# Performance work log

Measured on AMD Instinct MI355X. Metric: run time of the kernel, lower is better.

The kernel has to match this reference:

```python
import math
import jax, jax.numpy as jnp
import numpy as np

HEADS = 8

def relative_shift(score):
    # score: [B, H, S, 2S-1] -> [B, H, S, S] via Music Transformer skew trick
    B, H, S, R = score.shape
    score = jnp.pad(score, ((0, 0), (0, 0), (0, 0), (1, 0)))          # [B,H,S,2S]
    score = score.reshape(B, H, -1)[:, :, S:].reshape(B, H, S, -1)    # [B,H,S,2S-1]
    return score[..., :S]


def setup_inputs() -> dict:
    B, S, D = 4, 1024, 512
    dh = D // HEADS
    rng = jax.random.key(0)
    ks = jax.random.split(rng, 14)
    w = 0.02  # init scale
    return {
        "query":   jax.random.normal(ks[0], (B, S, D), jnp.float32),
        "key":     jax.random.normal(ks[1], (B, S, D), jnp.float32),
        "value":   jax.random.normal(ks[2], (B, S, D), jnp.float32),
        "pos_emb": jax.random.normal(ks[3], (2 * S - 1, dh), jnp.float32),
        "Wq": jax.random.normal(ks[4], (D, D), jnp.float32) * w,
        "bq": jnp.zeros((D,), jnp.float32),
        "Wk": jax.random.normal(ks[5], (D, D), jnp.float32) * w,
        "bk": jnp.zeros((D,), jnp.float32),
        "Wv": jax.random.normal(ks[6], (D, D), jnp.float32) * w,
        "bv": jnp.zeros((D,), jnp.float32),
        "Wo": jax.random.normal(ks[7], (D, D), jnp.float32) * w,
        "bo": jnp.zeros((D,), jnp.float32),
        "Wp": jax.random.normal(ks[8], (dh, dh), jnp.float32) * w,
        "bp": jnp.zeros((dh,), jnp.float32),
    }


def reference(query, key, value, pos_emb, Wq, bq, Wk, bk, Wv, bv, Wo, bo, Wp, bp):
    B, S, D = query.shape
    H = HEADS
    dh = D // H
    q = (query @ Wq.T + bq).reshape(B, S, H, dh).transpose(0, 2, 1, 3)  # [B,H,S,dh]
    k = (key   @ Wk.T + bk).reshape(B, S, H, dh).transpose(0, 2, 1, 3)  # [B,H,S,dh]
    v = (value @ Wv.T + bv).reshape(B, S, H, dh).transpose(0, 2, 1, 3)  # [B,H,S,dh]
    rel = pos_emb @ Wp.T + bp                                           # [2S-1, dh]

    pos_score = jnp.einsum('bhsd,rd->bhsr', q, rel)                     # [B,H,S,2S-1]
    pos_score = relative_shift(pos_score)                               # [B,H,S,S]
    content_score = jnp.einsum('bhsd,bhtd->bhst', q, k)                 # [B,H,S,S]
    score = (content_score + pos_score) / math.sqrt(D)                  # scale by sqrt(d_model)
    attn = jax.nn.softmax(score, axis=-1)
    out = jnp.einsum('bhst,bhtd->bshd', attn, v).reshape(B, S, D)
    return (out @ Wo.T + bo, attn, content_score, pos_score)
```

## Files before the change

### kernel.cpp

```cpp
#include <hip/hip_runtime.h>

typedef __attribute__((ext_vector_type(8))) short short8;
typedef __attribute__((ext_vector_type(4))) float f32x4;
typedef __attribute__((ext_vector_type(2))) float f32x2;
typedef unsigned short u16;
typedef unsigned int u32;

#define MFMA16(a, b, c) __builtin_amdgcn_mfma_f32_16x16x32_bf16((a), (b), (c), 0, 0, 0)
#define SCALE 0.044194173824159216f

#define SW(r, c) ((c) ^ (((r) & 7) << 3))

__device__ __forceinline__ u16 f2bf(float f) {
    u32 u = __float_as_uint(f);
    u = (u + 0x7fffu + ((u >> 16) & 1u)) >> 16;
    return (u16)u;
}

__global__ __launch_bounds__(256) void cvt_kernel(const float* __restrict__ src,
                                                  u16* __restrict__ dst, int n4) {
    int i = blockIdx.x * 256 + threadIdx.x;
    if (i >= n4) return;
    float4 v = ((const float4*)src)[i];
    unsigned long long p = (unsigned long long)f2bf(v.x)
                         | ((unsigned long long)f2bf(v.y) << 16)
                         | ((unsigned long long)f2bf(v.z) << 32)
                         | ((unsigned long long)f2bf(v.w) << 48);
    ((unsigned long long*)dst)[i] = p;
}

__global__ __launch_bounds__(256) void rel_kernel(const float* __restrict__ pos_emb,
                                                  const float* __restrict__ Wp,
                                                  const float* __restrict__ bp,
                                                  u16* __restrict__ rel) {
    int idx = blockIdx.x * 256 + threadIdx.x;
    if (idx >= 2047 * 64) return;
    int r = idx >> 6, c = idx & 63;
    const float* pe = pos_emb + r * 64;
    const float* w  = Wp + c * 64;
    float acc = bp[c];
#pragma unroll
    for (int k = 0; k < 64; k++) acc += pe[k] * w[k];
    rel[r * 64 + c] = f2bf(acc);
}

template <int MODE>
__global__ __launch_bounds__(256) void gemm_kernel(const u16* __restrict__ A,
                                                   const u16* __restrict__ B,
                                                   const float* __restrict__ bias,
                                                   void* __restrict__ Cout,
                                                   int M, int N, int K) {
    int tid = threadIdx.x;
    int w = tid >> 6, lane = tid & 63;
    int wi = w >> 1, wj = w & 1;
    int qd = lane >> 4, ln = lane & 15;
    int m_base = blockIdx.x * 64 + wi * 32;
    int n_base = blockIdx.y * 64 + wj * 32;
    f32x4 acc[2][2] = {};
    const u16* a0p = A + (long)(m_base + ln) * K + qd * 8;
    const u16* a1p = a0p + 16 * K;
    const u16* b0p = B + (long)(n_base + ln) * K + qd * 8;
    const u16* b1p = b0p + 16 * K;
    for (int kc = 0; kc < K; kc += 32) {
        short8 a0 = *(const short8*)(a0p + kc);
        short8 a1 = *(const short8*)(a1p + kc);
        short8 b0 = *(const short8*)(b0p + kc);
        short8 b1 = *(const short8*)(b1p + kc);
        acc[0][0] = MFMA16(a0, b0, acc[0][0]);
        acc[0][1] = MFMA16(a0, b1, acc[0][1]);
        acc[1][0] = MFMA16(a1, b0, acc[1][0]);
        acc[1][1] = MFMA16(a1, b1, acc[1][1]);
    }
#pragma unroll
    for (int i = 0; i < 2; i++)
#pragma unroll
        for (int j = 0; j < 2; j++)
#pragma unroll
            for (int r = 0; r < 4; r++) {
                int m = m_base + i * 16 + qd * 4 + r;
                int n = n_base + j * 16 + ln;
                float v = acc[i][j][r];
                if (MODE == 0) {
                    v += bias[n];
                    int b = m >> 10, s = m & 1023, h = n >> 6, d = n & 63;
                    ((u16*)Cout)[(((long)(b * 8 + h) << 10) + s) * 64 + d] = f2bf(v);
                } else if (MODE == 1) {
                    v += bias[m];
                    int b = n >> 10, t = n & 1023, h = m >> 6, d = m & 63;
                    ((u16*)Cout)[(((long)(b * 8 + h) * 64 + d) << 10) + t] = f2bf(v);
                } else {
                    v += bias[n];
                    ((float*)Cout)[(long)m * N + n] = v;
                }
            }
}

__global__ __launch_bounds__(256) void score_kernel(const u16* __restrict__ qws,
                                                    const u16* __restrict__ kws,
                                                    const u16* __restrict__ vtws,
                                                    const u16* __restrict__ relws,
                                                    float* __restrict__ out_attn,
                                                    float* __restrict__ out_cont,
                                                    float* __restrict__ out_pos,
                                                    u16* __restrict__ ctx,
                                                    float* __restrict__ sinvws) {
    __shared__ __align__(16) u16 sc[32][1024];
    int st = blockIdx.x, h = blockIdx.y, b = blockIdx.z;
    int s0 = st * 32;
    int tid = threadIdx.x;
    int w = tid >> 6, lane = tid & 63, qd = lane >> 4, ln = lane & 15;
    int bh = b * 8 + h;
    int c0 = w * 256;

    const u16* qbase  = qws + ((long)bh << 10) * 64;
    const u16* kbase  = kws + ((long)bh << 10) * 64;
    const u16* vtbase = vtws + ((long)bh << 6) * 1024;
    float* attn_base = out_attn + ((long)bh << 20) + (long)s0 * 1024;
    float* cont_base = out_cont + ((long)bh << 20) + (long)s0 * 1024;
    float* pos_base  = out_pos  + ((long)bh << 20) + (long)s0 * 1024;

    short8 qa00 = *(const short8*)(qbase + (s0 + ln) * 64 + qd * 8);
    short8 qa01 = *(const short8*)(qbase + (s0 + ln) * 64 + 32 + qd * 8);
    short8 qa10 = *(const short8*)(qbase + (s0 + 16 + ln) * 64 + qd * 8);
    short8 qa11 = *(const short8*)(qbase + (s0 + 16 + ln) * 64 + 32 + qd * 8);

    for (int tt = 0; tt < 16; tt++) {
        int t0 = c0 + tt * 16;
        const u16* kp = kbase + (t0 + ln) * 64 + qd * 8;
        short8 kb0 = *(const short8*)(kp);
        short8 kb1 = *(const short8*)(kp + 32);
        f32x4 a0 = {}, a1 = {};
        a0 = MFMA16(qa00, kb0, a0);
        a0 = MFMA16(qa01, kb1, a0);
        a1 = MFMA16(qa10, kb0, a1);
        a1 = MFMA16(qa11, kb1, a1);
        int t = t0 + ln;
#pragma unroll
        for (int r = 0; r < 4; r++) {
            int sl = qd * 4 + r;
            cont_base[sl * 1024 + t] = a0[r];
            cont_base[(sl + 16) * 1024 + t] = a1[r];
            sc[sl][SW(sl, t)] = f2bf(a0[r] * SCALE);
            sc[sl + 16][SW(sl + 16, t)] = f2bf(a1[r] * SCALE);
        }
    }

    int rbase = 1008 - s0;
    for (int rt = 16 * w - 1; rt <= 16 * w + 16; rt++) {
        int r0 = rbase + rt * 16;
        const u16* rp = relws + (r0 + ln) * 64 + qd * 8;
        short8 rb0 = *(const short8*)(rp);
        short8 rb1 = *(const short8*)(rp + 32);
        f32x4 a0 = {}, a1 = {};
        a0 = MFMA16(qa00, rb0, a0);
        a0 = MFMA16(qa01, rb1, a0);
        a1 = MFMA16(qa10, rb0, a1);
        a1 = MFMA16(qa11, rb1, a1);
#pragma unroll
        for (int r = 0; r < 4; r++) {
            int sl = qd * 4 + r;
            int t = rt * 16 + ln + sl - 15;
            if (t >= c0 && t < c0 + 256) {
                pos_base[sl * 1024 + t] = a0[r];
                u16 cur = sc[sl][SW(sl, t)];
                float fv = __uint_as_float((u32)cur << 16) + a0[r] * SCALE;
                sc[sl][SW(sl, t)] = f2bf(fv);
            }
            int t1 = t + 16;
            if (t1 >= c0 && t1 < c0 + 256) {
                pos_base[(sl + 16) * 1024 + t1] = a1[r];
                u16 cur = sc[sl + 16][SW(sl + 16, t1)];
                float fv = __uint_as_float((u32)cur << 16) + a1[r] * SCALE;
                sc[sl + 16][SW(sl + 16, t1)] = f2bf(fv);
            }
        }
    }
    __syncthreads();

    {
        int row = tid >> 3, g = tid & 7;
        float sum = 0.f;
#pragma unroll
        for (int i = 0; i < 64; i++) {
            int c = 2 * g + 16 * i;
            u32 pk = *(const u32*)&sc[row][SW(row, c)];
            float e0 = __expf(__uint_as_float(pk << 16));
            float e1 = __expf(__uint_as_float(pk & 0xffff0000u));
            sum += e0 + e1;
            u32 pe;
            asm("v_cvt_pk_bf16_f32 %0, %1, %2" : "=v"(pe) : "v"(e0), "v"(e1));
            *(u32*)&sc[row][SW(row, c)] = pe;
        }
        sum += __shfl_xor(sum, 1, 8);
        sum += __shfl_xor(sum, 2, 8);
        sum += __shfl_xor(sum, 4, 8);
        float inv = 1.0f / sum;
        if (g == 0) sinvws[((long)bh << 10) + s0 + row] = inv;
#pragma unroll
        for (int i = 0; i < 64; i++) {
            int c = 2 * g + 16 * i;
            u32 pk = *(const u32*)&sc[row][SW(row, c)];
            f32x2 av = {__uint_as_float(pk << 16) * inv,
                        __uint_as_float(pk & 0xffff0000u) * inv};
            *(f32x2*)&attn_base[row * 1024 + c] = av;
        }
    }
    __syncthreads();

    {
        float inv0[4], inv1[4];
#pragma unroll
        for (int r = 0; r < 4; r++) {
            inv0[r] = sinvws[((long)bh << 10) + s0 + qd * 4 + r];
            inv1[r] = sinvws[((long)bh << 10) + s0 + 16 + qd * 4 + r];
        }
        const u16* vrow = vtbase + (w * 16 + ln) * 1024 + qd * 8;
        f32x4 oa00 = {}, oa01 = {}, oa10 = {}, oa11 = {};
#pragma unroll
        for (int kt = 0; kt < 32; kt += 2) {
            int ca = kt * 32 + qd * 8;
            int cb = ca + 32;
            short8 a0  = *(const short8*)&sc[ln][SW(ln, ca)];
            short8 a1  = *(const short8*)&sc[ln + 16][SW(ln + 16, ca)];
            short8 b0  = *(const short8*)(vrow + kt * 32);
            short8 a0b = *(const short8*)&sc[ln][SW(ln, cb)];
            short8 a1b = *(const short8*)&sc[ln + 16][SW(ln + 16, cb)];
            short8 b1  = *(const short8*)(vrow + kt * 32 + 32);
            oa00 = MFMA16(a0, b0, oa00);
            oa10 = MFMA16(a1, b0, oa10);
            oa01 = MFMA16(a0b, b1, oa01);
            oa11 = MFMA16(a1b, b1, oa11);
        }
        int d = w * 16 + ln;
#pragma unroll
        for (int r = 0; r < 4; r++) {
            int sl = qd * 4 + r;
            ctx[((long)(b * 1024 + s0 + sl)) * 512 + h * 64 + d] =
                f2bf((oa00[r] + oa01[r]) * inv0[r]);
            ctx[((long)(b * 1024 + s0 + 16 + sl)) * 512 + h * 64 + d] =
                f2bf((oa10[r] + oa11[r]) * inv1[r]);
        }
    }
}

extern "C" void kernel_launch(void* const* d_in, const int* in_sizes, int n_in,
                              void* d_out, int out_size, void* d_ws, size_t ws_size,
                              hipStream_t stream) {
    (void)in_sizes; (void)n_in; (void)out_size; (void)ws_size;
    const float* query   = (const float*)d_in[0];
    const float* key     = (const float*)d_in[1];
    const float* value   = (const float*)d_in[2];
    const float* pos_emb = (const float*)d_in[3];
    const float* Wq = (const float*)d_in[4];
    const float* bq = (const float*)d_in[5];
    const float* Wk = (const float*)d_in[6];
    const float* bk = (const float*)d_in[7];
    const float* Wv = (const float*)d_in[8];
    const float* bv = (const float*)d_in[9];
    const float* Wo = (const float*)d_in[10];
    const float* bo = (const float*)d_in[11];
    const float* Wp = (const float*)d_in[12];
    const float* bp = (const float*)d_in[13];

    u16* qin  = (u16*)d_ws;
    u16* kin  = qin + 4096 * 512;
    u16* vin  = kin + 4096 * 512;
    u16* wqb  = vin + 4096 * 512;
    u16* wkb  = wqb + 512 * 512;
    u16* wvb  = wkb + 512 * 512;
    u16* wob  = wvb + 512 * 512;
    u16* relb = wob + 512 * 512;
    u16* qws  = relb + 2048 * 64;
    u16* kws  = qws + 4 * 8 * 1024 * 64;
    u16* vtws = kws + 4 * 8 * 1024 * 64;
    u16* ctx  = qin;
    float* sinvws = (float*)kin;

    float* out  = (float*)d_out;
    float* attn = out + 2097152;
    float* cont = attn + 33554432;
    float* pos  = cont + 33554432;

    cvt_kernel<<<2048, 256, 0, stream>>>(query, qin, 524288);
    cvt_kernel<<<2048, 256, 0, stream>>>(key, kin, 524288);
    cvt_kernel<<<2048, 256, 0, stream>>>(value, vin, 524288);
    cvt_kernel<<<256, 256, 0, stream>>>(Wq, wqb, 65536);
    cvt_kernel<<<256, 256, 0, stream>>>(Wk, wkb, 65536);
    cvt_kernel<<<256, 256, 0, stream>>>(Wv, wvb, 65536);
    cvt_kernel<<<256, 256, 0, stream>>>(Wo, wob, 65536);
    rel_kernel<<<512, 256, 0, stream>>>(pos_emb, Wp, bp, relb);

    gemm_kernel<0><<<dim3(64, 8), 256, 0, stream>>>(qin, wqb, bq, qws, 4096, 512, 512);
    gemm_kernel<0><<<dim3(64, 8), 256, 0, stream>>>(kin, wkb, bk, kws, 4096, 512, 512);
    gemm_kernel<1><<<dim3(8, 64), 256, 0, stream>>>(wvb, vin, bv, vtws, 512, 4096, 512);

    score_kernel<<<dim3(32, 8, 4), 256, 0, stream>>>(qws, kws, vtws, relb,
                                                     attn, cont, pos, ctx, sinvws);

    gemm_kernel<2><<<dim3(64, 8), 256, 0, stream>>>(ctx, wob, bo, out, 4096, 512, 512);
}
```

Baseline: 214.4 us.

## Double score kernel block to 512 threads and keep softmax inverses in LDS

The score kernel now runs 8 waves per block instead of 4, each covering 128 key columns rather than 256. The softmax pass uses 16 threads per row, and the PV matmul work is split across waves by row-half and head-dim slice. The per-row inverse sums now live in shared memory rather than a global workspace, which removes a global round-trip. The goal is more parallelism and latency hiding per block for the store-heavy kernel. In exchange, the relative-position halo tiles are recomputed more often because each wave's column slice is narrower.

Result: slower. 254.1 us (+18.6%).

```diff
diff --git a/kernel.cpp b/kernel.cpp
--- a/kernel.cpp
+++ b/kernel.cpp
@@ -95,22 +95,22 @@
             }
 }
 
-__global__ __launch_bounds__(256) void score_kernel(const u16* __restrict__ qws,
+__global__ __launch_bounds__(512) void score_kernel(const u16* __restrict__ qws,
                                                     const u16* __restrict__ kws,
                                                     const u16* __restrict__ vtws,
                                                     const u16* __restrict__ relws,
                                                     float* __restrict__ out_attn,
                                                     float* __restrict__ out_cont,
                                                     float* __restrict__ out_pos,
-                                                    u16* __restrict__ ctx,
-                                                    float* __restrict__ sinvws) {
+                                                    u16* __restrict__ ctx) {
     __shared__ __align__(16) u16 sc[32][1024];
+    __shared__ float sinv[32];
     int st = blockIdx.x, h = blockIdx.y, b = blockIdx.z;
     int s0 = st * 32;
     int tid = threadIdx.x;
     int w = tid >> 6, lane = tid & 63, qd = lane >> 4, ln = lane & 15;
     int bh = b * 8 + h;
-    int c0 = w * 256;
+    int c0 = w * 128;
 
     const u16* qbase  = qws + ((long)bh << 10) * 64;
     const u16* kbase  = kws + ((long)bh << 10) * 64;
@@ -124,7 +124,7 @@
     short8 qa10 = *(const short8*)(qbase + (s0 + 16 + ln) * 64 + qd * 8);
     short8 qa11 = *(const short8*)(qbase + (s0 + 16 + ln) * 64 + 32 + qd * 8);
 
-    for (int tt = 0; tt < 16; tt++) {
+    for (int tt = 0; tt < 8; tt++) {
         int t0 = c0 + tt * 16;
         const u16* kp = kbase + (t0 + ln) * 64 + qd * 8;
         short8 kb0 = *(const short8*)(kp);
@@ -146,7 +146,7 @@
     }
 
     int rbase = 1008 - s0;
-    for (int rt = 16 * w - 1; rt <= 16 * w + 16; rt++) {
+    for (int rt = 8 * w - 1; rt <= 8 * w + 8; rt++) {
         int r0 = rbase + rt * 16;
         const u16* rp = relws + (r0 + ln) * 64 + qd * 8;
         short8 rb0 = *(const short8*)(rp);
@@ -160,14 +160,14 @@
         for (int r = 0; r < 4; r++) {
             int sl = qd * 4 + r;
             int t = rt * 16 + ln + sl - 15;
-            if (t >= c0 && t < c0 + 256) {
+            if (t >= c0 && t < c0 + 128) {
                 pos_base[sl * 1024 + t] = a0[r];
                 u16 cur = sc[sl][SW(sl, t)];
                 float fv = __uint_as_float((u32)cur << 16) + a0[r] * SCALE;
                 sc[sl][SW(sl, t)] = f2bf(fv);
             }
             int t1 = t + 16;
-            if (t1 >= c0 && t1 < c0 + 256) {
+            if (t1 >= c0 && t1 < c0 + 128) {
                 pos_base[(sl + 16) * 1024 + t1] = a1[r];
                 u16 cur = sc[sl + 16][SW(sl + 16, t1)];
                 float fv = __uint_as_float((u32)cur << 16) + a1[r] * SCALE;
@@ -178,11 +178,11 @@
     __syncthreads();
 
     {
-        int row = tid >> 3, g = tid & 7;
+        int row = tid >> 4, g = tid & 15;
         float sum = 0.f;
 #pragma unroll
-        for (int i = 0; i < 64; i++) {
-            int c = 2 * g + 16 * i;
+        for (int i = 0; i < 32; i++) {
+            int c = 2 * g + 32 * i;
             u32 pk = *(const u32*)&sc[row][SW(row, c)];
             float e0 = __expf(__uint_as_float(pk << 16));
             float e1 = __expf(__uint_as_float(pk & 0xffff0000u));
@@ -191,14 +191,15 @@
             asm("v_cvt_pk_bf16_f32 %0, %1, %2" : "=v"(pe) : "v"(e0), "v"(e1));
             *(u32*)&sc[row][SW(row, c)] = pe;
         }
-        sum += __shfl_xor(sum, 1, 8);
-        sum += __shfl_xor(sum, 2, 8);
-        sum += __shfl_xor(sum, 4, 8);
+        sum += __shfl_xor(sum, 1, 16);
+        sum += __shfl_xor(sum, 2, 16);
+        sum += __shfl_xor(sum, 4, 16);
+        sum += __shfl_xor(sum, 8, 16);
         float inv = 1.0f / sum;
-        if (g == 0) sinvws[((long)bh << 10) + s0 + row] = inv;
-#pragma unroll
-        for (int i = 0; i < 64; i++) {
-            int c = 2 * g + 16 * i;
+        if (g == 0) sinv[row] = inv;
+#pragma unroll
+        for (int i = 0; i < 32; i++) {
+            int c = 2 * g + 32 * i;
             u32 pk = *(const u32*)&sc[row][SW(row, c)];
             f32x2 av = {__uint_as_float(pk << 16) * inv,
                         __uint_as_float(pk & 0xffff0000u) * inv};
@@ -208,37 +209,29 @@
     __syncthreads();
 
     {
-        float inv0[4], inv1[4];
-#pragma unroll
-        for (int r = 0; r < 4; r++) {
-            inv0[r] = sinvws[((long)bh << 10) + s0 + qd * 4 + r];
-            inv1[r] = sinvws[((long)bh << 10) + s0 + 16 + qd * 4 + r];
-        }
-        const u16* vrow = vtbase + (w * 16 + ln) * 1024 + qd * 8;
-        f32x4 oa00 = {}, oa01 = {}, oa10 = {}, oa11 = {};
+        int rt2 = (w & 1) * 16;
+        int d0 = (w >> 1) * 16;
+        float invv[4];
+#pragma unroll
+        for (int r = 0; r < 4; r++) invv[r] = sinv[rt2 + qd * 4 + r];
+        const u16* vrow = vtbase + (d0 + ln) * 1024 + qd * 8;
+        f32x4 oa0 = {}, oa1 = {};
 #pragma unroll
         for (int kt = 0; kt < 32; kt += 2) {
             int ca = kt * 32 + qd * 8;
-            int cb = ca + 32;
-            short8 a0  = *(const short8*)&sc[ln][SW(ln, ca)];
-            short8 a1  = *(const short8*)&sc[ln + 16][SW(ln + 16, ca)];
-            short8 b0  = *(const short8*)(vrow + kt * 32);
-            short8 a0b = *(const short8*)&sc[ln][SW(ln, cb)];
-            short8 a1b = *(const short8*)&sc[ln + 16][SW(ln + 16, cb)];
-            short8 b1  = *(const short8*)(vrow + kt * 32 + 32);
-            oa00 = MFMA16(a0, b0, oa00);
-            oa10 = MFMA16(a1, b0, oa10);
-            oa01 = MFMA16(a0b, b1, oa01);
-            oa11 = MFMA16(a1b, b1, oa11);
-        }
-        int d = w * 16 + ln;
+            short8 a0 = *(const short8*)&sc[rt2 + ln][SW(rt2 + ln, ca)];
+            short8 b0 = *(const short8*)(vrow + kt * 32);
+            short8 a1 = *(const short8*)&sc[rt2 + ln][SW(rt2 + ln, ca + 32)];
+            short8 b1 = *(const short8*)(vrow + kt * 32 + 32);
+            oa0 = MFMA16(a0, b0, oa0);
+            oa1 = MFMA16(a1, b1, oa1);
+        }
+        int d = d0 + ln;
 #pragma unroll
         for (int r = 0; r < 4; r++) {
-            int sl = qd * 4 + r;
+            int sl = rt2 + qd * 4 + r;
             ctx[((long)(b * 1024 + s0 + sl)) * 512 + h * 64 + d] =
-                f2bf((oa00[r] + oa01[r]) * inv0[r]);
-            ctx[((long)(b * 1024 + s0 + 16 + sl)) * 512 + h * 64 + d] =
-                f2bf((oa10[r] + oa11[r]) * inv1[r]);
+                f2bf((oa0[r] + oa1[r]) * invv[r]);
         }
     }
 }
@@ -274,7 +267,6 @@
     u16* kws  = qws + 4 * 8 * 1024 * 64;
     u16* vtws = kws + 4 * 8 * 1024 * 64;
     u16* ctx  = qin;
-    float* sinvws = (float*)kin;
 
     float* out  = (float*)d_out;
     float* attn = out + 2097152;
@@ -294,8 +286,8 @@
     gemm_kernel<0><<<dim3(64, 8), 256, 0, stream>>>(kin, wkb, bk, kws, 4096, 512, 512);
     gemm_kernel<1><<<dim3(8, 64), 256, 0, stream>>>(wvb, vin, bv, vtws, 512, 4096, 512);
 
-    score_kernel<<<dim3(32, 8, 4), 256, 0, stream>>>(qws, kws, vtws, relb,
-                                                     attn, cont, pos, ctx, sinvws);
+    score_kernel<<<dim3(32, 8, 4), 512, 0, stream>>>(qws, kws, vtws, relb,
+                                                     attn, cont, pos, ctx);
 
     gemm_kernel<2><<<dim3(64, 8), 256, 0, stream>>>(ctx, wob, bo, out, 4096, 512, 512);
 }
```
